# Kernel optimization log

Measured on AMD Instinct MI355X. Metric: run time of the kernel, lower is better.

## Reference

```python
import jax, jax.numpy as jnp
import numpy as np
from jax import lax


def setup_inputs() -> dict:
    key = jax.random.key(0)
    k1, k2, k3, k4 = jax.random.split(key, 4)
    N, D, B, R, EF = 100000, 256, 64, 32, 32
    storage = jax.random.normal(k1, (N, D), dtype=jnp.float32)
    query = jax.random.normal(k2, (B, D), dtype=jnp.float32)
    graph = jax.random.randint(k3, (N, R), 0, N, dtype=jnp.int32)      # fixed-degree NSW adjacency
    initial = jax.random.randint(k4, (B, EF), 0, N, dtype=jnp.int32)   # random entry points (entry())
    return {"query": query, "storage": storage, "graph": graph,
            "initial": initial, "k": 10, "ef_search": EF}


def reference(query, storage, graph, initial, k, ef_search):
    """Batched greedy best-first NSW search (ef_search fixed expansion steps)."""
    N = storage.shape[0]
    INF = jnp.float32(1e30)

    def sqdist(q, ids):
        diff = storage[ids] - q            # [R, D] gather
        return jnp.sum(diff * diff, axis=-1)

    def search_one(q, init):
        cd = sqdist(q, init)                               # candidate distances [EF]
        visited = jnp.zeros((N,), jnp.bool_).at[init].set(True)
        expanded = jnp.zeros((N,), jnp.bool_)

        def step(state, _):
            cid, cd, visited, expanded = state
            # pick closest unexpanded candidate
            pickd = jnp.where(expanded[cid], INF, cd)
            j = jnp.argmin(pickd)
            u = cid[j]
            expanded = expanded.at[u].set(True)
            # expand neighbors of u
            nbrs = graph[u]                                # [R]
            fresh = ~visited[nbrs]
            nd = jnp.where(fresh, sqdist(q, nbrs), INF)    # skip already-visited
            visited = visited.at[nbrs].set(True)
            # merge candidate pool, keep ef_search best
            all_ids = jnp.concatenate([cid, nbrs])
            all_d = jnp.concatenate([cd, nd])
            negd, idx = lax.top_k(-all_d, ef_search)
            return (all_ids[idx], -negd, visited, expanded), None

        (cid, cd, _, _), _ = lax.scan(step, (init, cd, visited, expanded),
                                      None, length=ef_search)
        negk, idx = lax.top_k(-cd, k)
        return cid[idx], -negk

    topk_ids, topk_dists = jax.vmap(search_one)(query, initial)
    return topk_ids, topk_dists
```

## Files before the change

### kernel.cpp

```cpp
#include <hip/hip_runtime.h>


#define DIMS   256
#define RDEG   32
#define EFPOOL 32
#define KOUT   10
#define NWORDS 3125
#define INF_D  1e30f

typedef unsigned long long u64;

__global__ __launch_bounds__(64, 1) void nsw_wave_kernel(
    const float* __restrict__ query,
    const float* __restrict__ storage,
    const int*   __restrict__ graph,
    const int*   __restrict__ initial,
    float*       __restrict__ out,
    int B)
{
    __shared__ unsigned int visited[NWORDS];
    __shared__ unsigned int expanded[NWORDS];
    __shared__ float4 qsh[DIMS / 4];
    __shared__ u64    keys[64];
    __shared__ float  sc_d[EFPOOL];
    __shared__ int    sc_id[EFPOOL];

    const int l    = threadIdx.x;
    const int b    = blockIdx.x;
    const int nb   = l & 31;
    const int half = l >> 5;

    for (int i = l; i < NWORDS; i += 64) { visited[i] = 0u; expanded[i] = 0u; }

    qsh[l] = reinterpret_cast<const float4*>(query + (size_t)b * DIMS)[l];

    float pool_d  = INF_D;
    int   pool_id = 0;
    int   u       = 0;
    int   nbid    = initial[b * EFPOOL + nb];

    if (l < 32) atomicOr(&visited[nbid >> 5], 1u << (nbid & 31));

    float4 r[32];
    {
        const float4* sp = reinterpret_cast<const float4*>(
            storage + (size_t)nbid * DIMS) + half * 32;
        #pragma unroll
        for (int j = 0; j < 32; ++j) r[j] = sp[j];
    }

    for (int s = 0; s <= EFPOOL; ++s) {
        if (s > 0 && l == 0) expanded[u >> 5] |= 1u << (u & 31);

        bool fresh = true;
        if (s > 0) {
            unsigned vw = visited[nbid >> 5];
            fresh = !((vw >> (nbid & 31)) & 1u);
            if ((l < 32) && fresh) atomicOr(&visited[nbid >> 5], 1u << (nbid & 31));
        }

        bool ounexp = !((expanded[pool_id >> 5] >> (pool_id & 31)) & 1u);
        u64  obm    = __ballot(ounexp && (l < 32));
        int  oslot  = (obm == 0ull) ? 0 : (__ffsll(obm) - 1);
        float old_d = __shfl(pool_d,  oslot, 64);
        int   old_id= __shfl(pool_id, oslot, 64);
        bool  old_ok= (obm != 0ull);

        float a0 = 0.f, a1 = 0.f, a2 = 0.f, a3 = 0.f;
        #pragma unroll
        for (int j = 0; j < 32; ++j) {
            float4 q = qsh[half * 32 + j];
            float d0 = r[j].x - q.x; a0 = fmaf(d0, d0, a0);
            float d1 = r[j].y - q.y; a1 = fmaf(d1, d1, a1);
            float d2 = r[j].z - q.z; a2 = fmaf(d2, d2, a2);
            float d3 = r[j].w - q.w; a3 = fmaf(d3, d3, a3);
        }
        float part = (a0 + a1) + (a2 + a3);
        float d  = part + __shfl_xor(part, 32, 64);
        float nd = fresh ? d : INF_D;

        int nnbid = nbid;
        int uspec = 0;
        if (s < EFPOOL) {
            u64 nk = fresh ? (((u64)__float_as_uint(nd) << 6) | (u64)(32 + nb))
                           : ~0ull;
            #pragma unroll
            for (int m = 1; m < 64; m <<= 1) {
                u64 o = __shfl_xor(nk, m, 64);
                nk = (o < nk) ? o : nk;
            }
            int new_id = __shfl(nbid, ((int)(nk & 63) - 32) & 31, 64);
            u64 ok = old_ok ? (((u64)__float_as_uint(old_d) << 6) | (u64)oslot)
                            : ~0ull;
            uspec = (ok < nk) ? old_id : new_id;
            nnbid = graph[(size_t)uspec * RDEG + nb];
        }

        {
            float ed  = half ? nd   : pool_d;
            int   eid = half ? nbid : pool_id;
            u64 key = ((u64)__float_as_uint(ed) << 6) | (unsigned)l;
            keys[l] = key;
            int rank = 0;
            #pragma unroll
            for (int j = 0; j < 64; ++j)
                rank += (keys[j] < key) ? 1 : 0;
            if (rank < EFPOOL) { sc_d[rank] = ed; sc_id[rank] = eid; }
            pool_d  = sc_d[nb];
            pool_id = sc_id[nb];
        }

        if (s < EFPOOL) {
            bool unexp = !((expanded[pool_id >> 5] >> (pool_id & 31)) & 1u);
            u64 bm = __ballot(unexp && (l < 32));
            int slot = (bm == 0ull) ? 0 : (__ffsll(bm) - 1);
            int utrue = sc_id[slot];
            int ut = __builtin_amdgcn_readfirstlane(utrue);
            int us = __builtin_amdgcn_readfirstlane(uspec);
            if (ut != us)
                nnbid = graph[(size_t)utrue * RDEG + nb];
            u    = utrue;
            nbid = nnbid;
            const float4* sp = reinterpret_cast<const float4*>(
                storage + (size_t)nbid * DIMS) + half * 32;
            #pragma unroll
            for (int j = 0; j < 32; ++j) r[j] = sp[j];
        }
    }

    if (l < KOUT) {
        out[b * KOUT + l]            = (float)pool_id;
        out[B * KOUT + b * KOUT + l] = pool_d;
    }
}

extern "C" void kernel_launch(void* const* d_in, const int* in_sizes, int n_in,
                              void* d_out, int out_size, void* d_ws, size_t ws_size,
                              hipStream_t stream) {
    const float* query   = (const float*)d_in[0];
    const float* storage = (const float*)d_in[1];
    const int*   graph   = (const int*)d_in[2];
    const int*   initial = (const int*)d_in[3];
    float* out = (float*)d_out;

    const int B = in_sizes[0] / DIMS;

    nsw_wave_kernel<<<B, 64, 0, stream>>>(query, storage, graph, initial, out, B);
}
```

Measured before the change: 228.2 us.

## Prefetch graph row of best old candidate and overlap storage fill with merge

Loads the adjacency row of the best unexpanded pool entry before the distance computation, so it is ready if that entry wins. When the old candidate wins, the storage row fill for its neighbours is issued before the pool merge, hiding that latency behind the rank sort. If the true pick differs, the fill is reissued. The min-reduction now runs over 32 lanes instead of 64. This adds an extra graph load per step and code divergence between the two branches.

```diff
diff --git a/kernel.cpp b/kernel.cpp
--- a/kernel.cpp
+++ b/kernel.cpp
@@ -42,12 +42,36 @@
     if (l < 32) atomicOr(&visited[nbid >> 5], 1u << (nbid & 31));
 
     float4 r[32];
-    {
+
+    auto issue_fill = [&](int id) {
         const float4* sp = reinterpret_cast<const float4*>(
-            storage + (size_t)nbid * DIMS) + half * 32;
+            storage + (size_t)id * DIMS) + half * 32;
         #pragma unroll
         for (int j = 0; j < 32; ++j) r[j] = sp[j];
-    }
+    };
+
+    auto do_merge = [&](float nd_) {
+        float ed  = half ? nd_  : pool_d;
+        int   eid = half ? nbid : pool_id;
+        u64 key = ((u64)__float_as_uint(ed) << 6) | (unsigned)l;
+        keys[l] = key;
+        int rank = 0;
+        #pragma unroll
+        for (int j = 0; j < 64; ++j)
+            rank += (keys[j] < key) ? 1 : 0;
+        if (rank < EFPOOL) { sc_d[rank] = ed; sc_id[rank] = eid; }
+        pool_d  = sc_d[nb];
+        pool_id = sc_id[nb];
+    };
+
+    auto true_pick = [&]() -> int {
+        bool unexp = !((expanded[pool_id >> 5] >> (pool_id & 31)) & 1u);
+        u64 bm = __ballot(unexp && (l < 32));
+        int slot = (bm == 0ull) ? 0 : (__ffsll(bm) - 1);
+        return sc_id[slot];
+    };
+
+    issue_fill(nbid);
 
     for (int s = 0; s <= EFPOOL; ++s) {
         if (s > 0 && l == 0) expanded[u >> 5] |= 1u << (u & 31);
@@ -65,6 +89,9 @@
         float old_d = __shfl(pool_d,  oslot, 64);
         int   old_id= __shfl(pool_id, oslot, 64);
         bool  old_ok= (obm != 0ull);
+        int   gpre  = 0;
+        if (s < EFPOOL)
+            gpre = graph[(size_t)old_id * RDEG + nb];
 
         float a0 = 0.f, a1 = 0.f, a2 = 0.f, a3 = 0.f;
         #pragma unroll
@@ -79,52 +106,44 @@
         float d  = part + __shfl_xor(part, 32, 64);
         float nd = fresh ? d : INF_D;
 
-        int nnbid = nbid;
-        int uspec = 0;
-        if (s < EFPOOL) {
-            u64 nk = fresh ? (((u64)__float_as_uint(nd) << 6) | (u64)(32 + nb))
-                           : ~0ull;
-            #pragma unroll
-            for (int m = 1; m < 64; m <<= 1) {
-                u64 o = __shfl_xor(nk, m, 64);
-                nk = (o < nk) ? o : nk;
+        if (s == EFPOOL) { do_merge(nd); break; }
+
+        u64 nk = fresh ? (((u64)__float_as_uint(nd) << 6) | (u64)(32 + nb))
+                       : ~0ull;
+        #pragma unroll
+        for (int m = 1; m < 32; m <<= 1) {
+            u64 o = __shfl_xor(nk, m, 64);
+            nk = (o < nk) ? o : nk;
+        }
+        int wslot = ((int)(nk & 63) - 32) & 31;
+        int new_id = __shfl(nbid, wslot, 64);
+        u64 okey = old_ok ? (((u64)__float_as_uint(old_d) << 6) | (u64)oslot)
+                          : ~0ull;
+        bool newwins = nk < okey;
+        int uspec, nnbid;
+
+        if (newwins) {
+            uspec = new_id;
+            nnbid = graph[(size_t)uspec * RDEG + nb];
+            do_merge(nd);
+            int utrue = true_pick();
+            if (__builtin_amdgcn_readfirstlane(utrue) !=
+                __builtin_amdgcn_readfirstlane(uspec))
+                nnbid = graph[(size_t)utrue * RDEG + nb];
+            u = utrue; nbid = nnbid;
+            issue_fill(nbid);
+        } else {
+            uspec = old_id;
+            nnbid = gpre;
+            issue_fill(nnbid);
+            do_merge(nd);
+            int utrue = true_pick();
+            if (__builtin_amdgcn_readfirstlane(utrue) !=
+                __builtin_amdgcn_readfirstlane(uspec)) {
+                nnbid = graph[(size_t)utrue * RDEG + nb];
+                issue_fill(nnbid);
             }
-            int new_id = __shfl(nbid, ((int)(nk & 63) - 32) & 31, 64);
-            u64 ok = old_ok ? (((u64)__float_as_uint(old_d) << 6) | (u64)oslot)
-                            : ~0ull;
-            uspec = (ok < nk) ? old_id : new_id;
-            nnbid = graph[(size_t)uspec * RDEG + nb];
-        }
-
-        {
-            float ed  = half ? nd   : pool_d;
-            int   eid = half ? nbid : pool_id;
-            u64 key = ((u64)__float_as_uint(ed) << 6) | (unsigned)l;
-            keys[l] = key;
-            int rank = 0;
-            #pragma unroll
-            for (int j = 0; j < 64; ++j)
-                rank += (keys[j] < key) ? 1 : 0;
-            if (rank < EFPOOL) { sc_d[rank] = ed; sc_id[rank] = eid; }
-            pool_d  = sc_d[nb];
-            pool_id = sc_id[nb];
-        }
-
-        if (s < EFPOOL) {
-            bool unexp = !((expanded[pool_id >> 5] >> (pool_id & 31)) & 1u);
-            u64 bm = __ballot(unexp && (l < 32));
-            int slot = (bm == 0ull) ? 0 : (__ffsll(bm) - 1);
-            int utrue = sc_id[slot];
-            int ut = __builtin_amdgcn_readfirstlane(utrue);
-            int us = __builtin_amdgcn_readfirstlane(uspec);
-            if (ut != us)
-                nnbid = graph[(size_t)utrue * RDEG + nb];
-            u    = utrue;
-            nbid = nnbid;
-            const float4* sp = reinterpret_cast<const float4*>(
-                storage + (size_t)nbid * DIMS) + half * 32;
-            #pragma unroll
-            for (int j = 0; j < 32; ++j) r[j] = sp[j];
+            u = utrue; nbid = nnbid;
         }
     }
 
```

Result: slower. 247.3 us (+8.3%).

## Add helper waves that prefetch neighbor rows via global_load_lds into cache

Applied to the files above, without the earlier changes.

Grows each block from one wave to four. Wave 0 runs the search and publishes each step's neighbor ids through shared memory with an atomic counter. The other three waves spin on that counter and issue global_load_lds touches of the neighbor storage rows, aiming to warm the cache before wave 0 issues its own loads. The change also prefetches the graph row of the best old candidate speculatively and shortens the shuffle min-reduction to 32 lanes. Risks include spin-wait overhead, a race where helpers read xnb while wave 0 overwrites it, and touches that arrive no earlier than wave 0's own loads.

```diff
diff --git a/kernel.cpp b/kernel.cpp
--- a/kernel.cpp
+++ b/kernel.cpp
@@ -7,10 +7,11 @@
 #define KOUT   10
 #define NWORDS 3125
 #define INF_D  1e30f
+#define NPUB   33
 
 typedef unsigned long long u64;
 
-__global__ __launch_bounds__(64, 1) void nsw_wave_kernel(
+__global__ __launch_bounds__(256, 1) void nsw_wave_kernel(
     const float* __restrict__ query,
     const float* __restrict__ storage,
     const int*   __restrict__ graph,
@@ -24,13 +25,47 @@
     __shared__ u64    keys[64];
     __shared__ float  sc_d[EFPOOL];
     __shared__ int    sc_id[EFPOOL];
-
-    const int l    = threadIdx.x;
+    __shared__ int    xnb[EFPOOL];
+    __shared__ int    xcnt;
+    __shared__ float4 touchpad[64];
+
+    const int t    = threadIdx.x;
+    const int wv   = t >> 6;
+    const int l    = t & 63;
     const int b    = blockIdx.x;
     const int nb   = l & 31;
     const int half = l >> 5;
 
-    for (int i = l; i < NWORDS; i += 64) { visited[i] = 0u; expanded[i] = 0u; }
+    for (int i = t; i < NWORDS; i += 256) { visited[i] = 0u; expanded[i] = 0u; }
+    if (t == 0) xcnt = 0;
+    __syncthreads();
+
+    if (wv != 0) {
+        const int h     = wv - 1;
+        const int start = h * 86;
+        const int count = (h == 2) ? 84 : 86;
+        for (int pub = 1; pub <= NPUB; ++pub) {
+            while (__hip_atomic_load(&xcnt, __ATOMIC_RELAXED,
+                                     __HIP_MEMORY_SCOPE_WORKGROUP) < pub)
+                __builtin_amdgcn_s_sleep(1);
+            #pragma unroll
+            for (int i = 0; i < 2; ++i) {
+                int idx = i * 64 + l;
+                if (idx < count) {
+                    int line = start + idx;
+                    const char* src = (const char*)storage
+                        + (size_t)xnb[line >> 3] * (DIMS * sizeof(float))
+                        + (size_t)(line & 7) * 128;
+                    __builtin_amdgcn_global_load_lds(
+                        (const __attribute__((address_space(1))) void*)src,
+                        (__attribute__((address_space(3))) void*)&touchpad[0],
+                        16, 0, 0);
+                }
+            }
+        }
+        asm volatile("s_waitcnt vmcnt(0)" ::: "memory");
+        return;
+    }
 
     qsh[l] = reinterpret_cast<const float4*>(query + (size_t)b * DIMS)[l];
 
@@ -40,6 +75,11 @@
     int   nbid    = initial[b * EFPOOL + nb];
 
     if (l < 32) atomicOr(&visited[nbid >> 5], 1u << (nbid & 31));
+
+    int pub = 1;
+    if (l < 32) xnb[nb] = nbid;
+    if (l == 0) __hip_atomic_store(&xcnt, pub, __ATOMIC_RELAXED,
+                                   __HIP_MEMORY_SCOPE_WORKGROUP);
 
     float4 r[32];
     {
@@ -65,6 +105,9 @@
         float old_d = __shfl(pool_d,  oslot, 64);
         int   old_id= __shfl(pool_id, oslot, 64);
         bool  old_ok= (obm != 0ull);
+        int   gpre  = 0;
+        if (s < EFPOOL)
+            gpre = graph[(size_t)old_id * RDEG + nb];
 
         float a0 = 0.f, a1 = 0.f, a2 = 0.f, a3 = 0.f;
         #pragma unroll
@@ -85,15 +128,18 @@
             u64 nk = fresh ? (((u64)__float_as_uint(nd) << 6) | (u64)(32 + nb))
                            : ~0ull;
             #pragma unroll
-            for (int m = 1; m < 64; m <<= 1) {
+            for (int m = 1; m < 32; m <<= 1) {
                 u64 o = __shfl_xor(nk, m, 64);
                 nk = (o < nk) ? o : nk;
             }
-            int new_id = __shfl(nbid, ((int)(nk & 63) - 32) & 31, 64);
-            u64 ok = old_ok ? (((u64)__float_as_uint(old_d) << 6) | (u64)oslot)
-                            : ~0ull;
-            uspec = (ok < nk) ? old_id : new_id;
-            nnbid = graph[(size_t)uspec * RDEG + nb];
+            int wslot  = ((int)(nk & 63) - 32) & 31;
+            int new_id = __shfl(nbid, wslot, 64);
+            u64 okey = old_ok ? (((u64)__float_as_uint(old_d) << 6) | (u64)oslot)
+                              : ~0ull;
+            bool newwins = nk < okey;
+            uspec = newwins ? new_id : old_id;
+            if (newwins) nnbid = graph[(size_t)uspec * RDEG + nb];
+            else         nnbid = gpre;
         }
 
         {
@@ -115,12 +161,17 @@
             u64 bm = __ballot(unexp && (l < 32));
             int slot = (bm == 0ull) ? 0 : (__ffsll(bm) - 1);
             int utrue = sc_id[slot];
-            int ut = __builtin_amdgcn_readfirstlane(utrue);
-            int us = __builtin_amdgcn_readfirstlane(uspec);
-            if (ut != us)
+            if (__builtin_amdgcn_readfirstlane(utrue) !=
+                __builtin_amdgcn_readfirstlane(uspec))
                 nnbid = graph[(size_t)utrue * RDEG + nb];
             u    = utrue;
             nbid = nnbid;
+
+            ++pub;
+            if (l < 32) xnb[nb] = nbid;
+            if (l == 0) __hip_atomic_store(&xcnt, pub, __ATOMIC_RELAXED,
+                                           __HIP_MEMORY_SCOPE_WORKGROUP);
+
             const float4* sp = reinterpret_cast<const float4*>(
                 storage + (size_t)nbid * DIMS) + half * 32;
             #pragma unroll
@@ -145,5 +196,5 @@
 
     const int B = in_sizes[0] / DIMS;
 
-    nsw_wave_kernel<<<B, 64, 0, stream>>>(query, storage, graph, initial, out, B);
+    nsw_wave_kernel<<<B, 256, 0, stream>>>(query, storage, graph, initial, out, B);
 }
```

Result: no change. 232.7 us (+2.0%).

## Split neighbor distance computation across four waves with LDS flag handoff

Applied to the files above, without the earlier changes.

Each block now runs four waves instead of one. Wave 0 keeps the pool/visited bookkeeping, and the neighbor rows are split so each wave fetches and scores 8 neighbors through padded LDS staging. The waves hand off work through spin-waited workgroup-scope atomics: a signal word carries the step number and whether neighbor ids were published, and a done counter collects the partial distances. Graph rows are prefetched for the speculated expansion node. This spreads the 32 row gathers over more waves to raise memory-level parallelism per query, at the cost of spin-wait overhead and LDS round trips each step.

```diff
diff --git a/kernel.cpp b/kernel.cpp
--- a/kernel.cpp
+++ b/kernel.cpp
@@ -1,16 +1,17 @@
 #include <hip/hip_runtime.h>
 
 
-#define DIMS   256
-#define RDEG   32
-#define EFPOOL 32
-#define KOUT   10
-#define NWORDS 3125
-#define INF_D  1e30f
+#define DIMS    256
+#define RDEG    32
+#define EFPOOL  32
+#define KOUT    10
+#define NWORDS  3125
+#define INF_D   1e30f
+#define RSTRIDE 65
 
 typedef unsigned long long u64;
 
-__global__ __launch_bounds__(64, 1) void nsw_wave_kernel(
+__global__ __launch_bounds__(256, 1) void nsw_mw_kernel(
     const float* __restrict__ query,
     const float* __restrict__ storage,
     const int*   __restrict__ graph,
@@ -21,18 +22,74 @@
     __shared__ unsigned int visited[NWORDS];
     __shared__ unsigned int expanded[NWORDS];
     __shared__ float4 qsh[DIMS / 4];
+    __shared__ float4 ldsrows[4][8 * RSTRIDE];
     __shared__ u64    keys[64];
     __shared__ float  sc_d[EFPOOL];
     __shared__ int    sc_id[EFPOOL];
-
-    const int l    = threadIdx.x;
+    __shared__ int    pub_ids[EFPOOL];
+    __shared__ float  dvals[EFPOOL];
+    __shared__ int    sig;
+    __shared__ int    uidsh;
+    __shared__ int    done;
+
+    const int t    = threadIdx.x;
+    const int wv   = t >> 6;
+    const int l    = t & 63;
     const int b    = blockIdx.x;
     const int nb   = l & 31;
     const int half = l >> 5;
-
-    for (int i = l; i < NWORDS; i += 64) { visited[i] = 0u; expanded[i] = 0u; }
-
-    qsh[l] = reinterpret_cast<const float4*>(query + (size_t)b * DIMS)[l];
+    const int fr   = l >> 3;
+    const int fl   = l & 7;
+    const int cr   = l & 7;
+    const bool act = (nb < 8);
+
+    for (int i = t; i < NWORDS; i += 256) { visited[i] = 0u; expanded[i] = 0u; }
+    if (t == 0) { sig = 0; done = 0; }
+    if (wv == 0)
+        qsh[l] = reinterpret_cast<const float4*>(query + (size_t)b * DIMS)[l];
+    __syncthreads();
+
+    if (wv != 0) {
+        for (int s = 0; s <= EFPOOL; ++s) {
+            int v;
+            do {
+                v = __hip_atomic_load(&sig, __ATOMIC_ACQUIRE,
+                                      __HIP_MEMORY_SCOPE_WORKGROUP);
+            } while ((v >> 1) != s + 1);
+            int gid;
+            if (v & 1) gid = pub_ids[wv * 8 + fr];
+            else       gid = graph[(size_t)uidsh * RDEG + wv * 8 + fr];
+
+            const float4* sp = reinterpret_cast<const float4*>(
+                storage + (size_t)gid * DIMS);
+            float4 rr[8];
+            #pragma unroll
+            for (int k = 0; k < 8; ++k) rr[k] = sp[fl * 8 + k];
+            #pragma unroll
+            for (int k = 0; k < 8; ++k)
+                ldsrows[wv][fr * RSTRIDE + fl * 8 + k] = rr[k];
+
+            float a0 = 0.f, a1 = 0.f, a2 = 0.f, a3 = 0.f;
+            if (act) {
+                #pragma unroll
+                for (int j = 0; j < 32; ++j) {
+                    float4 rv = ldsrows[wv][cr * RSTRIDE + half * 32 + j];
+                    float4 qv = qsh[half * 32 + j];
+                    float d0 = rv.x - qv.x; a0 = fmaf(d0, d0, a0);
+                    float d1 = rv.y - qv.y; a1 = fmaf(d1, d1, a1);
+                    float d2 = rv.z - qv.z; a2 = fmaf(d2, d2, a2);
+                    float d3 = rv.w - qv.w; a3 = fmaf(d3, d3, a3);
+                }
+            }
+            float part = (a0 + a1) + (a2 + a3);
+            float dd = part + __shfl_xor(part, 32, 64);
+            if (l < 8) dvals[wv * 8 + cr] = dd;
+            if (l == 0)
+                __hip_atomic_fetch_add(&done, 1, __ATOMIC_RELEASE,
+                                       __HIP_MEMORY_SCOPE_WORKGROUP);
+        }
+        return;
+    }
 
     float pool_d  = INF_D;
     int   pool_id = 0;
@@ -41,60 +98,60 @@
 
     if (l < 32) atomicOr(&visited[nbid >> 5], 1u << (nbid & 31));
 
-    float4 r[32];
-    {
+    if (l < 32) pub_ids[nb] = nbid;
+    if (l == 0) uidsh = 0;
+    __hip_atomic_store(&sig, (1 << 1) | 1, __ATOMIC_RELEASE,
+                       __HIP_MEMORY_SCOPE_WORKGROUP);
+
+    for (int s = 0; s <= EFPOOL; ++s) {
+        int gid = __shfl(nbid, fr, 64);
         const float4* sp = reinterpret_cast<const float4*>(
-            storage + (size_t)nbid * DIMS) + half * 32;
+            storage + (size_t)gid * DIMS);
+        float4 rr[8];
         #pragma unroll
-        for (int j = 0; j < 32; ++j) r[j] = sp[j];
-    }
-
-    for (int s = 0; s <= EFPOOL; ++s) {
+        for (int k = 0; k < 8; ++k) rr[k] = sp[fl * 8 + k];
+
         if (s > 0 && l == 0) expanded[u >> 5] |= 1u << (u & 31);
-
         bool fresh = true;
         if (s > 0) {
             unsigned vw = visited[nbid >> 5];
             fresh = !((vw >> (nbid & 31)) & 1u);
             if ((l < 32) && fresh) atomicOr(&visited[nbid >> 5], 1u << (nbid & 31));
         }
-
         bool ounexp = !((expanded[pool_id >> 5] >> (pool_id & 31)) & 1u);
         u64  obm    = __ballot(ounexp && (l < 32));
         int  oslot  = (obm == 0ull) ? 0 : (__ffsll(obm) - 1);
-        float old_d = __shfl(pool_d,  oslot, 64);
-        int   old_id= __shfl(pool_id, oslot, 64);
-        bool  old_ok= (obm != 0ull);
-
+        int  old_id = __shfl(pool_id, oslot, 64);
+        int  gpre   = 0;
+        if (s < EFPOOL)
+            gpre = graph[(size_t)old_id * RDEG + nb];
+
+        #pragma unroll
+        for (int k = 0; k < 8; ++k)
+            ldsrows[0][fr * RSTRIDE + fl * 8 + k] = rr[k];
         float a0 = 0.f, a1 = 0.f, a2 = 0.f, a3 = 0.f;
-        #pragma unroll
-        for (int j = 0; j < 32; ++j) {
-            float4 q = qsh[half * 32 + j];
-            float d0 = r[j].x - q.x; a0 = fmaf(d0, d0, a0);
-            float d1 = r[j].y - q.y; a1 = fmaf(d1, d1, a1);
-            float d2 = r[j].z - q.z; a2 = fmaf(d2, d2, a2);
-            float d3 = r[j].w - q.w; a3 = fmaf(d3, d3, a3);
+        if (act) {
+            #pragma unroll
+            for (int j = 0; j < 32; ++j) {
+                float4 rv = ldsrows[0][cr * RSTRIDE + half * 32 + j];
+                float4 qv = qsh[half * 32 + j];
+                float d0 = rv.x - qv.x; a0 = fmaf(d0, d0, a0);
+                float d1 = rv.y - qv.y; a1 = fmaf(d1, d1, a1);
+                float d2 = rv.z - qv.z; a2 = fmaf(d2, d2, a2);
+                float d3 = rv.w - qv.w; a3 = fmaf(d3, d3, a3);
+            }
         }
         float part = (a0 + a1) + (a2 + a3);
-        float d  = part + __shfl_xor(part, 32, 64);
-        float nd = fresh ? d : INF_D;
-
-        int nnbid = nbid;
-        int uspec = 0;
-        if (s < EFPOOL) {
-            u64 nk = fresh ? (((u64)__float_as_uint(nd) << 6) | (u64)(32 + nb))
-                           : ~0ull;
-            #pragma unroll
-            for (int m = 1; m < 64; m <<= 1) {
-                u64 o = __shfl_xor(nk, m, 64);
-                nk = (o < nk) ? o : nk;
-            }
-            int new_id = __shfl(nbid, ((int)(nk & 63) - 32) & 31, 64);
-            u64 ok = old_ok ? (((u64)__float_as_uint(old_d) << 6) | (u64)oslot)
-                            : ~0ull;
-            uspec = (ok < nk) ? old_id : new_id;
-            nnbid = graph[(size_t)uspec * RDEG + nb];
-        }
+        float dd = part + __shfl_xor(part, 32, 64);
+        if (l < 8) dvals[cr] = dd;
+        if (l == 0)
+            __hip_atomic_fetch_add(&done, 1, __ATOMIC_RELEASE,
+                                   __HIP_MEMORY_SCOPE_WORKGROUP);
+
+        while (__hip_atomic_load(&done, __ATOMIC_ACQUIRE,
+                                 __HIP_MEMORY_SCOPE_WORKGROUP) < 4 * (s + 1)) {}
+        float dm = dvals[nb];
+        float nd = fresh ? dm : INF_D;
 
         {
             float ed  = half ? nd   : pool_d;
@@ -115,16 +172,20 @@
             u64 bm = __ballot(unexp && (l < 32));
             int slot = (bm == 0ull) ? 0 : (__ffsll(bm) - 1);
             int utrue = sc_id[slot];
-            int ut = __builtin_amdgcn_readfirstlane(utrue);
-            int us = __builtin_amdgcn_readfirstlane(uspec);
-            if (ut != us)
-                nnbid = graph[(size_t)utrue * RDEG + nb];
-            u    = utrue;
-            nbid = nnbid;
-            const float4* sp = reinterpret_cast<const float4*>(
-                storage + (size_t)nbid * DIMS) + half * 32;
-            #pragma unroll
-            for (int j = 0; j < 32; ++j) r[j] = sp[j];
+            bool m1 = (__builtin_amdgcn_readfirstlane(utrue) ==
+                       __builtin_amdgcn_readfirstlane(old_id));
+            u = utrue;
+            if (m1) {
+                nbid = gpre;
+                if (l < 32) pub_ids[nb] = nbid;
+                __hip_atomic_store(&sig, ((s + 2) << 1) | 1, __ATOMIC_RELEASE,
+                                   __HIP_MEMORY_SCOPE_WORKGROUP);
+            } else {
+                if (l == 0) uidsh = utrue;
+                __hip_atomic_store(&sig, ((s + 2) << 1) | 0, __ATOMIC_RELEASE,
+                                   __HIP_MEMORY_SCOPE_WORKGROUP);
+                nbid = graph[(size_t)utrue * RDEG + nb];
+            }
         }
     }
 
@@ -145,5 +206,5 @@
 
     const int B = in_sizes[0] / DIMS;
 
-    nsw_wave_kernel<<<B, 64, 0, stream>>>(query, storage, graph, initial, out, B);
+    nsw_mw_kernel<<<B, 256, 0, stream>>>(query, storage, graph, initial, out, B);
 }
```

Result: slower. 263.1 us (+15.3%).
